# Kernel optimization log

Measured on AMD Instinct MI355X. Metric: run time of the kernel, lower is better.

Reference implementation:

```python
import jax, jax.numpy as jnp
import numpy as np

B, L, C = 2, 512, 64
EPS = 1e-5

def layer_norm(x, w, b):
    mu = jnp.mean(x, axis=-1, keepdims=True)
    var = jnp.mean(jnp.square(x - mu), axis=-1, keepdims=True)
    return (x - mu) * jax.lax.rsqrt(var + EPS) * w + b

def setup_inputs() -> dict:
    key = jax.random.key(0)
    ks = jax.random.split(key, 16)
    s = 1.0 / np.sqrt(C)
    def lin(k):
        k1, k2 = jax.random.split(k)
        return (jax.random.uniform(k1, (C, C), jnp.float32, -s, s),
                jax.random.uniform(k2, (C,), jnp.float32, -s, s))
    W_lp, b_lp = lin(ks[0]); W_rp, b_rp = lin(ks[1])
    W_lg, b_lg = lin(ks[2]); W_rg, b_rg = lin(ks[3])
    W_og, b_og = lin(ks[4]); W_out, b_out = lin(ks[5])
    return {
        'pairwise_states': jax.random.normal(ks[6], (B, L, L, C), jnp.float32),
        'attention_mask': jnp.ones((B, 1, 1, L), jnp.float32),
        'ln_in_w': jnp.ones((C,), jnp.float32), 'ln_in_b': jnp.zeros((C,), jnp.float32),
        'W_lp': W_lp, 'b_lp': b_lp, 'W_rp': W_rp, 'b_rp': b_rp,
        'W_lg': W_lg, 'b_lg': b_lg, 'W_rg': W_rg, 'b_rg': b_rg,
        'W_og': W_og, 'b_og': b_og,
        'ln_out_w': jnp.ones((C,), jnp.float32), 'ln_out_b': jnp.zeros((C,), jnp.float32),
        'W_out': W_out, 'b_out': b_out,
    }

def reference(pairwise_states, attention_mask, ln_in_w, ln_in_b,
              W_lp, b_lp, W_rp, b_rp, W_lg, b_lg, W_rg, b_rg,
              W_og, b_og, ln_out_w, ln_out_b, W_out, b_out):
    residual = pairwise_states
    x = layer_norm(pairwise_states, ln_in_w, ln_in_b)  # [B,L,L,C]
    left = x @ W_lp + b_lp
    right = x @ W_rp + b_rp
    # attention_mask [B,1,1,L].transpose(1,3) -> [B,L,1,1]: masks the i (row) axis
    m = jnp.transpose(attention_mask, (0, 3, 2, 1))
    left = left * m
    right = right * m
    left = left * jax.nn.sigmoid(x @ W_lg + b_lg)
    right = right * jax.nn.sigmoid(x @ W_rg + b_rg)
    out_gate = jax.nn.sigmoid(x @ W_og + b_og)
    # outgoing triangle update: out[b,i,j,c] = sum_k left[b,i,k,c] * right[b,j,k,c]
    tri = jnp.einsum('bikc,bjkc->bijc', left, right)
    y = layer_norm(tri, ln_out_w, ln_out_b) * out_gate
    y = y @ W_out + b_out
    return y + residual
```

## Files before the change

kernel.cpp:

```cpp
#include <hip/hip_runtime.h>
#include <cstdint>

typedef float f32x4 __attribute__((ext_vector_type(4)));
typedef short s16x8 __attribute__((ext_vector_type(8)));

#define APAD 72

__device__ __forceinline__ unsigned short f2bf(float f) {
  union { float f; uint32_t u; } v; v.f = f;
  uint32_t u = v.u;
  u += 0x7fffu + ((u >> 16) & 1u);
  return (unsigned short)(u >> 16);
}
__device__ __forceinline__ float bf2f(unsigned short h) {
  union { uint32_t u; float f; } v; v.u = ((uint32_t)h) << 16;
  return v.f;
}
__device__ __forceinline__ uint32_t pkbf(float a, float b) {
  uint32_t r;
  asm("v_cvt_pk_bf16_f32 %0, %1, %2" : "=v"(r) : "v"(a), "v"(b));
  return r;
}
__device__ __forceinline__ float sigmoidf_(float x) {
  return 1.0f / (1.0f + __expf(-x));
}
__device__ __forceinline__ f32x4 zero4() {
  f32x4 z = {0.f, 0.f, 0.f, 0.f};
  return z;
}
__device__ __forceinline__ void gl_lds16(const void* g, void* l) {
  __builtin_amdgcn_global_load_lds(
      (const __attribute__((address_space(1))) uint32_t*)g,
      (__attribute__((address_space(3))) uint32_t*)l, 16, 0, 0);
}

__global__ __launch_bounds__(256) void k_prep(
    const float* __restrict__ Wlp, const float* __restrict__ Wrp,
    const float* __restrict__ Wlg, const float* __restrict__ Wrg,
    const float* __restrict__ Wog, const float* __restrict__ Wout,
    unsigned short* __restrict__ wt) {
  const float* srcs[6] = {Wlp, Wrp, Wlg, Wrg, Wog, Wout};
  const int m = blockIdx.x;
  const float* W = srcs[m];
  const int t = threadIdx.x;
  for (int e = t; e < 64 * APAD; e += 256) {
    const int n = e / APAD, k = e - n * APAD;
    wt[m * (64 * APAD) + e] = (k < 64) ? f2bf(W[k * 64 + n]) : (unsigned short)0;
  }
}

__global__ __launch_bounds__(256, 4) void k1_proj(
    const float* __restrict__ xin, const float* __restrict__ mask,
    const float* __restrict__ lnw, const float* __restrict__ lnb,
    const float* __restrict__ blp, const float* __restrict__ brp,
    const float* __restrict__ blg, const float* __restrict__ brg,
    const unsigned short* __restrict__ wt,
    unsigned short* __restrict__ leftT, unsigned short* __restrict__ rightT) {
  __shared__ unsigned short A[64 * APAD];
  __shared__ unsigned short TL[64 * APAD];
  __shared__ unsigned short TR[64 * APAD];
  const int tid = threadIdx.x, lane = tid & 63, w = tid >> 6;
  const int bid = blockIdx.x;
  const int b = bid >> 12;
  const int i = (bid >> 3) & 511;
  const int k0 = (bid & 7) << 6;

  const int pair = w >> 1, ch = w & 1;
  const int kh8 = (lane >> 4) << 3;
  s16x8 wp[2][2], wg[2][2];
  float bPv[2], bGv[2];
  {
    const unsigned short* wtP = wt + (size_t)pair * (64 * APAD);
    const unsigned short* wtG = wt + (size_t)(2 + pair) * (64 * APAD);
    const float* bP = pair ? brp : blp;
    const float* bG = pair ? brg : blg;
#pragma unroll
    for (int nf2 = 0; nf2 < 2; ++nf2) {
      const int n = ch * 32 + nf2 * 16 + (lane & 15);
      const unsigned short* pp = wtP + n * APAD + kh8;
      const unsigned short* pg = wtG + n * APAD + kh8;
      wp[nf2][0] = *(const s16x8*)pp;  wp[nf2][1] = *(const s16x8*)(pp + 32);
      wg[nf2][0] = *(const s16x8*)pg;  wg[nf2][1] = *(const s16x8*)(pg + 32);
      bPv[nf2] = bP[n];  bGv[nf2] = bG[n];
    }
  }

  const int p = tid >> 2, q = tid & 3;
  const float* xrow = xin + (((size_t)b * 512 + i) * 512 + k0 + p) * 64 + q * 16;
  f32x4 xv[4];
#pragma unroll
  for (int u = 0; u < 4; ++u) xv[u] = ((const f32x4*)xrow)[u];
  float s1 = 0.f, s2 = 0.f;
#pragma unroll
  for (int u = 0; u < 4; ++u)
#pragma unroll
    for (int e = 0; e < 4; ++e) { float t = xv[u][e]; s1 += t; s2 += t * t; }
  s1 += __shfl_xor(s1, 1); s2 += __shfl_xor(s2, 1);
  s1 += __shfl_xor(s1, 2); s2 += __shfl_xor(s2, 2);
  const float mu = s1 * 0.015625f;
  const float rs = rsqrtf(s2 * 0.015625f - mu * mu + 1e-5f);
  {
    uint32_t pk[8];
#pragma unroll
    for (int u = 0; u < 4; ++u) {
      f32x4 wv = ((const f32x4*)(lnw + q * 16))[u];
      f32x4 bv = ((const f32x4*)(lnb + q * 16))[u];
#pragma unroll
      for (int e2 = 0; e2 < 2; ++e2) {
        pk[u * 2 + e2] = pkbf((xv[u][2 * e2] - mu) * rs * wv[2 * e2] + bv[2 * e2],
                              (xv[u][2 * e2 + 1] - mu) * rs * wv[2 * e2 + 1] + bv[2 * e2 + 1]);
      }
    }
    uint32_t* a32 = (uint32_t*)&A[p * APAD + q * 16];
#pragma unroll
    for (int u = 0; u < 8; ++u) a32[u] = pk[u];
  }
  const float mval = mask[b * 512 + i];
  __syncthreads();

  const int fr4 = (lane >> 4) << 2;
  unsigned short* T = pair ? TR : TL;
#pragma unroll
  for (int mf = 0; mf < 4; ++mf) {
    const int ar = (mf * 16 + (lane & 15)) * APAD + kh8;
    const s16x8 a0 = *(const s16x8*)&A[ar];
    const s16x8 a1 = *(const s16x8*)&A[ar + 32];
    f32x4 accP[2], accG[2];
#pragma unroll
    for (int nf2 = 0; nf2 < 2; ++nf2) {
      accP[nf2] = zero4(); accG[nf2] = zero4();
      accP[nf2] = __builtin_amdgcn_mfma_f32_16x16x32_bf16(a0, wp[nf2][0], accP[nf2], 0, 0, 0);
      accP[nf2] = __builtin_amdgcn_mfma_f32_16x16x32_bf16(a1, wp[nf2][1], accP[nf2], 0, 0, 0);
      accG[nf2] = __builtin_amdgcn_mfma_f32_16x16x32_bf16(a0, wg[nf2][0], accG[nf2], 0, 0, 0);
      accG[nf2] = __builtin_amdgcn_mfma_f32_16x16x32_bf16(a1, wg[nf2][1], accG[nf2], 0, 0, 0);
    }
    const int prow = mf * 16 + fr4;
#pragma unroll
    for (int nf2 = 0; nf2 < 2; ++nf2) {
      const int n = ch * 32 + nf2 * 16 + (lane & 15);
      const float bl = bPv[nf2], bg = bGv[nf2];
      float v0 = (accP[nf2][0] + bl) * mval * sigmoidf_(accG[nf2][0] + bg);
      float v1 = (accP[nf2][1] + bl) * mval * sigmoidf_(accG[nf2][1] + bg);
      float v2 = (accP[nf2][2] + bl) * mval * sigmoidf_(accG[nf2][2] + bg);
      float v3 = (accP[nf2][3] + bl) * mval * sigmoidf_(accG[nf2][3] + bg);
      *(uint32_t*)&T[n * APAD + prow] = pkbf(v0, v1);
      *(uint32_t*)&T[n * APAD + prow + 2] = pkbf(v2, v3);
    }
  }
  __syncthreads();

  {
    const int sn = tid >> 2, sq = tid & 3;
    const size_t gbase = (((size_t)b * 64 + sn) * 512 + i) * 512 + k0 + sq * 16;
    const uint32_t* sl = (const uint32_t*)&TL[sn * APAD + sq * 16];
    const uint32_t* sr = (const uint32_t*)&TR[sn * APAD + sq * 16];
    uint32_t* dl = (uint32_t*)(leftT + gbase);
    uint32_t* dr = (uint32_t*)(rightT + gbase);
#pragma unroll
    for (int u = 0; u < 8; ++u) dl[u] = sl[u];
#pragma unroll
    for (int u = 0; u < 8; ++u) dr[u] = sr[u];
  }
}

__global__ __launch_bounds__(256, 4) void k2_gemm(
    const unsigned short* __restrict__ leftT,
    const unsigned short* __restrict__ rightT,
    unsigned short* __restrict__ triT) {
  __shared__ __align__(16) unsigned short S[4 * 4096];
  const int tid = threadIdx.x, lane = tid & 63, w = tid >> 6;
  const int bid = blockIdx.x;
  const int sw = ((bid & 7) << 8) | (bid >> 3);
  const int plane = sw >> 4, tile = sw & 15;
  const size_t pb = (size_t)plane * 262144;
  const int i0 = (tile >> 2) << 7, j0 = (tile & 3) << 7;
  const int srow = lane >> 2;
  const int sk = (((lane & 3) ^ ((lane >> 2) & 3)) << 3);

  f32x4 acc[4][4];
#pragma unroll
  for (int mf = 0; mf < 4; ++mf)
#pragma unroll
    for (int nf = 0; nf < 4; ++nf) acc[mf][nf] = zero4();
  const int wr = (w >> 1) << 6, wc = (w & 1) << 6;

  auto stage = [&](int buf, int kt) {
    const int kk = kt << 5;
#pragma unroll
    for (int it = 0; it < 2; ++it) {
      const int ch = it * 4 + w;
      const int row = (ch << 4) + srow;
      gl_lds16(leftT + pb + (size_t)(i0 + row) * 512 + kk + sk,
               (char*)S + buf * 16384 + ch * 1024 + lane * 16);
      gl_lds16(rightT + pb + (size_t)(j0 + row) * 512 + kk + sk,
               (char*)S + buf * 16384 + 8192 + ch * 1024 + lane * 16);
    }
  };

  stage(0, 0);
  const int l15 = lane & 15;
  const int kosw = ((lane >> 4) ^ (lane & 3)) << 3;
  for (int kt = 0; kt < 16; ++kt) {
    __syncthreads();
    if (kt < 15) stage((kt & 1) ^ 1, kt + 1);
    const unsigned short* Ac = S + (kt & 1) * 8192;
    const unsigned short* Bc = Ac + 4096;
    s16x8 af[4], bfr[4];
#pragma unroll
    for (int mf = 0; mf < 4; ++mf)
      af[mf] = *(const s16x8*)&Ac[(wr + mf * 16 + l15) * 32 + kosw];
#pragma unroll
    for (int nf = 0; nf < 4; ++nf)
      bfr[nf] = *(const s16x8*)&Bc[(wc + nf * 16 + l15) * 32 + kosw];
#pragma unroll
    for (int mf = 0; mf < 4; ++mf)
#pragma unroll
      for (int nf = 0; nf < 4; ++nf)
        acc[mf][nf] = __builtin_amdgcn_mfma_f32_16x16x32_bf16(af[mf], bfr[nf], acc[mf][nf], 0, 0, 0);
  }
  __syncthreads();
  unsigned short* Tt = S;
#pragma unroll
  for (int mf = 0; mf < 4; ++mf)
#pragma unroll
    for (int nf = 0; nf < 4; ++nf) {
      const int col = wc + nf * 16 + l15;
#pragma unroll
      for (int r = 0; r < 4; ++r) {
        const int row = wr + mf * 16 + ((lane >> 4) << 2) + r;
        Tt[row * 128 + col] = f2bf(acc[mf][nf][r]);
      }
    }
  __syncthreads();
  {
    const int row = tid >> 1, half = (tid & 1) << 6;
    const uint32_t* src = (const uint32_t*)&Tt[row * 128 + half];
    uint32_t* dst = (uint32_t*)(triT + pb + (size_t)(i0 + row) * 512 + j0 + half);
#pragma unroll
    for (int u = 0; u < 32; ++u) dst[u] = src[u];
  }
}

#define OPAD 68
__global__ __launch_bounds__(256, 4) void k3_out(
    const unsigned short* __restrict__ triT,
    const float* __restrict__ resid,
    const float* __restrict__ lnw1, const float* __restrict__ lnb1,
    const float* __restrict__ bog,
    const float* __restrict__ lnw2, const float* __restrict__ lnb2,
    const float* __restrict__ bout,
    const unsigned short* __restrict__ wt,
    float* __restrict__ outp) {
  __shared__ __align__(16) unsigned char smem[36864];
  unsigned short* WTog  = (unsigned short*)smem;
  unsigned short* WTout = (unsigned short*)(smem + 9216);
  unsigned short* Y     = (unsigned short*)(smem + 18432);
  unsigned short* X     = (unsigned short*)(smem + 27648);
  float* OUT32 = (float*)(smem + 18432);
  const int tid = threadIdx.x, lane = tid & 63, w = tid >> 6;
  const int bid = blockIdx.x;
  const int b = bid >> 12;
  const int i = (bid >> 3) & 511;
  const int j0 = (bid & 7) << 6;

  {
    const char* wsrc = (const char*)(wt + (size_t)4 * (64 * APAD));
#pragma unroll
    for (int it = 0; it < 5; ++it) {
      const int off = (it * 256 + tid) * 16;
      if (off < 18432) gl_lds16(wsrc + off, (char*)WTog + off);
    }
  }

  const int j = tid >> 2, q = tid & 3;
  {
    const int c = tid >> 2;
    const int csw = c ^ (q << 4);
    const size_t srow = ((size_t)(b * 64 + c) * 512 + i) * 512 + j0 + q * 16;
    union { uint32_t u32[8]; unsigned short s[16]; } uu;
    const uint32_t* s32 = (const uint32_t*)(triT + srow);
#pragma unroll
    for (int u = 0; u < 8; ++u) uu.u32[u] = s32[u];
#pragma unroll
    for (int s = 0; s < 16; ++s) Y[(q * 16 + s) * APAD + csw] = uu.s[s];
  }
  f32x4 rv[4];
  {
    const float* rrow = resid + (((size_t)b * 512 + i) * 512 + j0 + j) * 64 + q * 16;
#pragma unroll
    for (int u = 0; u < 4; ++u) rv[u] = ((const f32x4*)rrow)[u];
    float s1 = 0.f, s2 = 0.f;
#pragma unroll
    for (int u = 0; u < 4; ++u)
#pragma unroll
      for (int e = 0; e < 4; ++e) { float t = rv[u][e]; s1 += t; s2 += t * t; }
    s1 += __shfl_xor(s1, 1); s2 += __shfl_xor(s2, 1);
    s1 += __shfl_xor(s1, 2); s2 += __shfl_xor(s2, 2);
    const float mu = s1 * 0.015625f;
    const float rs = rsqrtf(s2 * 0.015625f - mu * mu + 1e-5f);
    uint32_t pk[8];
#pragma unroll
    for (int u = 0; u < 4; ++u) {
      f32x4 wv = ((const f32x4*)(lnw1 + q * 16))[u];
      f32x4 bv = ((const f32x4*)(lnb1 + q * 16))[u];
#pragma unroll
      for (int e2 = 0; e2 < 2; ++e2) {
        pk[u * 2 + e2] = pkbf((rv[u][2 * e2] - mu) * rs * wv[2 * e2] + bv[2 * e2],
                              (rv[u][2 * e2 + 1] - mu) * rs * wv[2 * e2 + 1] + bv[2 * e2 + 1]);
      }
    }
    uint32_t* x32 = (uint32_t*)&X[j * APAD + q * 16];
#pragma unroll
    for (int u = 0; u < 8; ++u) x32[u] = pk[u];
  }
  __syncthreads();

  const int l15 = lane & 15, hi = lane >> 4;
  const int jrow = w * 16 + l15;
  const int ybase = jrow * APAD;
  const int kh8 = hi << 3;
  float yv[16];
#pragma unroll
  for (int nf = 0; nf < 4; ++nf) {
    const int pc = (((nf ^ w) & 3) << 4) + (hi << 2);
    const uint2 dd = *(const uint2*)&Y[ybase + pc];
    yv[nf * 4 + 0] = bf2f((unsigned short)(dd.x & 0xffff));
    yv[nf * 4 + 1] = bf2f((unsigned short)(dd.x >> 16));
    yv[nf * 4 + 2] = bf2f((unsigned short)(dd.y & 0xffff));
    yv[nf * 4 + 3] = bf2f((unsigned short)(dd.y >> 16));
  }
  float t1 = 0.f, t2 = 0.f;
#pragma unroll
  for (int s = 0; s < 16; ++s) { t1 += yv[s]; t2 += yv[s] * yv[s]; }
  t1 += __shfl_xor(t1, 16); t2 += __shfl_xor(t2, 16);
  t1 += __shfl_xor(t1, 32); t2 += __shfl_xor(t2, 32);
  const float mu2 = t1 * 0.015625f;
  const float rs2 = rsqrtf(t2 * 0.015625f - mu2 * mu2 + 1e-5f);

  float sg[16];
  {
    const s16x8 xb0 = *(const s16x8*)&X[ybase + kh8];
    const s16x8 xb1 = *(const s16x8*)&X[ybase + kh8 + 32];
#pragma unroll
    for (int nf = 0; nf < 4; ++nf) {
      const int wrow = (nf * 16 + l15) * APAD + kh8;
      const s16x8 wa0 = *(const s16x8*)&WTog[wrow];
      const s16x8 wa1 = *(const s16x8*)&WTog[wrow + 32];
      f32x4 aog = zero4();
      aog = __builtin_amdgcn_mfma_f32_16x16x32_bf16(wa0, xb0, aog, 0, 0, 0);
      aog = __builtin_amdgcn_mfma_f32_16x16x32_bf16(wa1, xb1, aog, 0, 0, 0);
      const f32x4 bb4 = *(const f32x4*)(bog + nf * 16 + (hi << 2));
      sg[nf * 4 + 0] = sigmoidf_(aog[0] + bb4[0]);
      sg[nf * 4 + 1] = sigmoidf_(aog[1] + bb4[1]);
      sg[nf * 4 + 2] = sigmoidf_(aog[2] + bb4[2]);
      sg[nf * 4 + 3] = sigmoidf_(aog[3] + bb4[3]);
    }
  }
#pragma unroll
  for (int nf = 0; nf < 4; ++nf) {
    const f32x4 wv = *(const f32x4*)(lnw2 + nf * 16 + (hi << 2));
    const f32x4 bv = *(const f32x4*)(lnb2 + nf * 16 + (hi << 2));
    const float y0 = ((yv[nf * 4 + 0] - mu2) * rs2 * wv[0] + bv[0]) * sg[nf * 4 + 0];
    const float y1 = ((yv[nf * 4 + 1] - mu2) * rs2 * wv[1] + bv[1]) * sg[nf * 4 + 1];
    const float y2 = ((yv[nf * 4 + 2] - mu2) * rs2 * wv[2] + bv[2]) * sg[nf * 4 + 2];
    const float y3 = ((yv[nf * 4 + 3] - mu2) * rs2 * wv[3] + bv[3]) * sg[nf * 4 + 3];
    uint2 o;
    o.x = pkbf(y0, y1);
    o.y = pkbf(y2, y3);
    const int pc = (((nf ^ w) & 3) << 4) + (hi << 2);
    *(uint2*)&Y[ybase + pc] = o;
  }
  __syncthreads();

  {
    const int xsw = (w & 3) << 4;
    const s16x8 a0 = *(const s16x8*)&Y[ybase + (kh8 ^ xsw)];
    const s16x8 a1 = *(const s16x8*)&Y[ybase + ((32 + kh8) ^ xsw)];
    s16x8 wb0[4], wb1[4];
#pragma unroll
    for (int nf = 0; nf < 4; ++nf) {
      const int brow = (nf * 16 + l15) * APAD + kh8;
      wb0[nf] = *(const s16x8*)&WTout[brow];
      wb1[nf] = *(const s16x8*)&WTout[brow + 32];
    }
    __syncthreads();
    f32x4 ao[4];
#pragma unroll
    for (int nf = 0; nf < 4; ++nf) {
      ao[nf] = zero4();
      ao[nf] = __builtin_amdgcn_mfma_f32_16x16x32_bf16(a0, wb0[nf], ao[nf], 0, 0, 0);
      ao[nf] = __builtin_amdgcn_mfma_f32_16x16x32_bf16(a1, wb1[nf], ao[nf], 0, 0, 0);
    }
#pragma unroll
    for (int nf = 0; nf < 4; ++nf) {
      const int n = nf * 16 + l15;
      const float bo = bout[n];
#pragma unroll
      for (int r = 0; r < 4; ++r) {
        const int prow = w * 16 + (hi << 2) + r;
        OUT32[prow * OPAD + n] = ao[nf][r] + bo;
      }
    }
  }
  __syncthreads();

  {
    const size_t gb = (((size_t)b * 512 + i) * 512 + j0 + j) * 64 + q * 16;
    float* op = outp + gb;
#pragma unroll
    for (int u = 0; u < 4; ++u) {
      f32x4 ov = ((const f32x4*)&OUT32[j * OPAD + q * 16])[u];
      ((f32x4*)op)[u] = ov + rv[u];
    }
  }
}

extern "C" void kernel_launch(void* const* d_in, const int* in_sizes, int n_in,
                              void* d_out, int out_size, void* d_ws, size_t ws_size,
                              hipStream_t stream) {
  const float* x     = (const float*)d_in[0];
  const float* mask  = (const float*)d_in[1];
  const float* lnw1  = (const float*)d_in[2];
  const float* lnb1  = (const float*)d_in[3];
  const float* Wlp   = (const float*)d_in[4];
  const float* blp   = (const float*)d_in[5];
  const float* Wrp   = (const float*)d_in[6];
  const float* brp   = (const float*)d_in[7];
  const float* Wlg   = (const float*)d_in[8];
  const float* blg   = (const float*)d_in[9];
  const float* Wrg   = (const float*)d_in[10];
  const float* brg   = (const float*)d_in[11];
  const float* Wog   = (const float*)d_in[12];
  const float* bog   = (const float*)d_in[13];
  const float* lnw2  = (const float*)d_in[14];
  const float* lnb2  = (const float*)d_in[15];
  const float* Wout  = (const float*)d_in[16];
  const float* bout  = (const float*)d_in[17];

  unsigned short* leftT  = (unsigned short*)d_ws;
  unsigned short* rightT = leftT + (size_t)33554432;
  unsigned short* triT   = rightT + (size_t)33554432;
  unsigned short* wt     = triT + (size_t)33554432;

  k_prep<<<6, 256, 0, stream>>>(Wlp, Wrp, Wlg, Wrg, Wog, Wout, wt);
  k1_proj<<<8192, 256, 0, stream>>>(x, mask, lnw1, lnb1, blp, brp, blg, brg,
                                    wt, leftT, rightT);
  k2_gemm<<<2048, 256, 0, stream>>>(leftT, rightT, triT);
  k3_out<<<8192, 256, 0, stream>>>(triT, x, lnw1, lnb1, bog, lnw2, lnb2, bout,
                                   wt, (float*)d_out);
}
```

Before: 242.5 us.

## Keep k3 LN-input in registers and write output directly from MFMA fragments

The output kernel now computes the input layernorm straight into MFMA B-fragment registers instead of staging X through shared memory. It swaps the output GEMM operand order so results land in row-major fragments that can be written to global memory directly, which removes the OUT32 shared buffer and two barriers. Shared memory drops from 36KB to 27KB and launch bounds rise to 5 blocks per SM for higher occupancy. The cost is that the residual is read from global twice, and the final stores are 16-byte chunks per lane rather than full contiguous rows.

```diff
diff --git a/kernel.cpp b/kernel.cpp
--- a/kernel.cpp
+++ b/kernel.cpp
@@ -241,8 +241,7 @@
   }
 }
 
-#define OPAD 68
-__global__ __launch_bounds__(256, 4) void k3_out(
+__global__ __launch_bounds__(256, 5) void k3_out(
     const unsigned short* __restrict__ triT,
     const float* __restrict__ resid,
     const float* __restrict__ lnw1, const float* __restrict__ lnb1,
@@ -251,12 +250,10 @@
     const float* __restrict__ bout,
     const unsigned short* __restrict__ wt,
     float* __restrict__ outp) {
-  __shared__ __align__(16) unsigned char smem[36864];
+  __shared__ __align__(16) unsigned char smem[27648];
   unsigned short* WTog  = (unsigned short*)smem;
   unsigned short* WTout = (unsigned short*)(smem + 9216);
   unsigned short* Y     = (unsigned short*)(smem + 18432);
-  unsigned short* X     = (unsigned short*)(smem + 27648);
-  float* OUT32 = (float*)(smem + 18432);
   const int tid = threadIdx.x, lane = tid & 63, w = tid >> 6;
   const int bid = blockIdx.x;
   const int b = bid >> 12;
@@ -272,7 +269,50 @@
     }
   }
 
-  const int j = tid >> 2, q = tid & 3;
+  const int l15 = lane & 15, hi = lane >> 4;
+  const int jrow = w * 16 + l15;
+  const size_t rowbase = (((size_t)b * 512 + i) * 512 + j0 + jrow) * 64;
+  const int kh8 = hi << 3;
+
+  s16x8 xb0, xb1;
+  {
+    f32x4 rx[4];
+    rx[0] = *(const f32x4*)(resid + rowbase + kh8);
+    rx[1] = *(const f32x4*)(resid + rowbase + kh8 + 4);
+    rx[2] = *(const f32x4*)(resid + rowbase + 32 + kh8);
+    rx[3] = *(const f32x4*)(resid + rowbase + 36 + kh8);
+    float s1 = 0.f, s2 = 0.f;
+#pragma unroll
+    for (int u = 0; u < 4; ++u)
+#pragma unroll
+      for (int e = 0; e < 4; ++e) { float t = rx[u][e]; s1 += t; s2 += t * t; }
+    s1 += __shfl_xor(s1, 16); s2 += __shfl_xor(s2, 16);
+    s1 += __shfl_xor(s1, 32); s2 += __shfl_xor(s2, 32);
+    const float mu = s1 * 0.015625f;
+    const float rs = rsqrtf(s2 * 0.015625f - mu * mu + 1e-5f);
+    union { uint32_t u[4]; s16x8 v; } p0, p1;
+#pragma unroll
+    for (int u = 0; u < 2; ++u) {
+      f32x4 wv = *(const f32x4*)(lnw1 + kh8 + u * 4);
+      f32x4 bv = *(const f32x4*)(lnb1 + kh8 + u * 4);
+      p0.u[u * 2 + 0] = pkbf((rx[u][0] - mu) * rs * wv[0] + bv[0],
+                             (rx[u][1] - mu) * rs * wv[1] + bv[1]);
+      p0.u[u * 2 + 1] = pkbf((rx[u][2] - mu) * rs * wv[2] + bv[2],
+                             (rx[u][3] - mu) * rs * wv[3] + bv[3]);
+    }
+#pragma unroll
+    for (int u = 0; u < 2; ++u) {
+      f32x4 wv = *(const f32x4*)(lnw1 + 32 + kh8 + u * 4);
+      f32x4 bv = *(const f32x4*)(lnb1 + 32 + kh8 + u * 4);
+      p1.u[u * 2 + 0] = pkbf((rx[u + 2][0] - mu) * rs * wv[0] + bv[0],
+                             (rx[u + 2][1] - mu) * rs * wv[1] + bv[1]);
+      p1.u[u * 2 + 1] = pkbf((rx[u + 2][2] - mu) * rs * wv[2] + bv[2],
+                             (rx[u + 2][3] - mu) * rs * wv[3] + bv[3]);
+    }
+    xb0 = p0.v; xb1 = p1.v;
+  }
+
+  const int q = tid & 3;
   {
     const int c = tid >> 2;
     const int csw = c ^ (q << 4);
@@ -284,41 +324,9 @@
 #pragma unroll
     for (int s = 0; s < 16; ++s) Y[(q * 16 + s) * APAD + csw] = uu.s[s];
   }
-  f32x4 rv[4];
-  {
-    const float* rrow = resid + (((size_t)b * 512 + i) * 512 + j0 + j) * 64 + q * 16;
-#pragma unroll
-    for (int u = 0; u < 4; ++u) rv[u] = ((const f32x4*)rrow)[u];
-    float s1 = 0.f, s2 = 0.f;
-#pragma unroll
-    for (int u = 0; u < 4; ++u)
-#pragma unroll
-      for (int e = 0; e < 4; ++e) { float t = rv[u][e]; s1 += t; s2 += t * t; }
-    s1 += __shfl_xor(s1, 1); s2 += __shfl_xor(s2, 1);
-    s1 += __shfl_xor(s1, 2); s2 += __shfl_xor(s2, 2);
-    const float mu = s1 * 0.015625f;
-    const float rs = rsqrtf(s2 * 0.015625f - mu * mu + 1e-5f);
-    uint32_t pk[8];
-#pragma unroll
-    for (int u = 0; u < 4; ++u) {
-      f32x4 wv = ((const f32x4*)(lnw1 + q * 16))[u];
-      f32x4 bv = ((const f32x4*)(lnb1 + q * 16))[u];
-#pragma unroll
-      for (int e2 = 0; e2 < 2; ++e2) {
-        pk[u * 2 + e2] = pkbf((rv[u][2 * e2] - mu) * rs * wv[2 * e2] + bv[2 * e2],
-                              (rv[u][2 * e2 + 1] - mu) * rs * wv[2 * e2 + 1] + bv[2 * e2 + 1]);
-      }
-    }
-    uint32_t* x32 = (uint32_t*)&X[j * APAD + q * 16];
-#pragma unroll
-    for (int u = 0; u < 8; ++u) x32[u] = pk[u];
-  }
-  __syncthreads();
-
-  const int l15 = lane & 15, hi = lane >> 4;
-  const int jrow = w * 16 + l15;
+  __syncthreads();
+
   const int ybase = jrow * APAD;
-  const int kh8 = hi << 3;
   float yv[16];
 #pragma unroll
   for (int nf = 0; nf < 4; ++nf) {
@@ -337,33 +345,21 @@
   const float mu2 = t1 * 0.015625f;
   const float rs2 = rsqrtf(t2 * 0.015625f - mu2 * mu2 + 1e-5f);
 
-  float sg[16];
-  {
-    const s16x8 xb0 = *(const s16x8*)&X[ybase + kh8];
-    const s16x8 xb1 = *(const s16x8*)&X[ybase + kh8 + 32];
-#pragma unroll
-    for (int nf = 0; nf < 4; ++nf) {
-      const int wrow = (nf * 16 + l15) * APAD + kh8;
-      const s16x8 wa0 = *(const s16x8*)&WTog[wrow];
-      const s16x8 wa1 = *(const s16x8*)&WTog[wrow + 32];
-      f32x4 aog = zero4();
-      aog = __builtin_amdgcn_mfma_f32_16x16x32_bf16(wa0, xb0, aog, 0, 0, 0);
-      aog = __builtin_amdgcn_mfma_f32_16x16x32_bf16(wa1, xb1, aog, 0, 0, 0);
-      const f32x4 bb4 = *(const f32x4*)(bog + nf * 16 + (hi << 2));
-      sg[nf * 4 + 0] = sigmoidf_(aog[0] + bb4[0]);
-      sg[nf * 4 + 1] = sigmoidf_(aog[1] + bb4[1]);
-      sg[nf * 4 + 2] = sigmoidf_(aog[2] + bb4[2]);
-      sg[nf * 4 + 3] = sigmoidf_(aog[3] + bb4[3]);
-    }
-  }
 #pragma unroll
   for (int nf = 0; nf < 4; ++nf) {
+    const int wrow = (nf * 16 + l15) * APAD + kh8;
+    const s16x8 wa0 = *(const s16x8*)&WTog[wrow];
+    const s16x8 wa1 = *(const s16x8*)&WTog[wrow + 32];
+    f32x4 aog = zero4();
+    aog = __builtin_amdgcn_mfma_f32_16x16x32_bf16(wa0, xb0, aog, 0, 0, 0);
+    aog = __builtin_amdgcn_mfma_f32_16x16x32_bf16(wa1, xb1, aog, 0, 0, 0);
+    const f32x4 bg4 = *(const f32x4*)(bog + nf * 16 + (hi << 2));
     const f32x4 wv = *(const f32x4*)(lnw2 + nf * 16 + (hi << 2));
     const f32x4 bv = *(const f32x4*)(lnb2 + nf * 16 + (hi << 2));
-    const float y0 = ((yv[nf * 4 + 0] - mu2) * rs2 * wv[0] + bv[0]) * sg[nf * 4 + 0];
-    const float y1 = ((yv[nf * 4 + 1] - mu2) * rs2 * wv[1] + bv[1]) * sg[nf * 4 + 1];
-    const float y2 = ((yv[nf * 4 + 2] - mu2) * rs2 * wv[2] + bv[2]) * sg[nf * 4 + 2];
-    const float y3 = ((yv[nf * 4 + 3] - mu2) * rs2 * wv[3] + bv[3]) * sg[nf * 4 + 3];
+    const float y0 = ((yv[nf * 4 + 0] - mu2) * rs2 * wv[0] + bv[0]) * sigmoidf_(aog[0] + bg4[0]);
+    const float y1 = ((yv[nf * 4 + 1] - mu2) * rs2 * wv[1] + bv[1]) * sigmoidf_(aog[1] + bg4[1]);
+    const float y2 = ((yv[nf * 4 + 2] - mu2) * rs2 * wv[2] + bv[2]) * sigmoidf_(aog[2] + bg4[2]);
+    const float y3 = ((yv[nf * 4 + 3] - mu2) * rs2 * wv[3] + bv[3]) * sigmoidf_(aog[3] + bg4[3]);
     uint2 o;
     o.x = pkbf(y0, y1);
     o.y = pkbf(y2, y3);
@@ -373,44 +369,24 @@
   __syncthreads();
 
   {
-    const int xsw = (w & 3) << 4;
+    const int xsw = w << 4;
     const s16x8 a0 = *(const s16x8*)&Y[ybase + (kh8 ^ xsw)];
     const s16x8 a1 = *(const s16x8*)&Y[ybase + ((32 + kh8) ^ xsw)];
-    s16x8 wb0[4], wb1[4];
+    f32x4 rv4[4];
+#pragma unroll
+    for (int nf = 0; nf < 4; ++nf)
+      rv4[nf] = *(const f32x4*)(resid + rowbase + nf * 16 + (hi << 2));
 #pragma unroll
     for (int nf = 0; nf < 4; ++nf) {
       const int brow = (nf * 16 + l15) * APAD + kh8;
-      wb0[nf] = *(const s16x8*)&WTout[brow];
-      wb1[nf] = *(const s16x8*)&WTout[brow + 32];
-    }
-    __syncthreads();
-    f32x4 ao[4];
-#pragma unroll
-    for (int nf = 0; nf < 4; ++nf) {
-      ao[nf] = zero4();
-      ao[nf] = __builtin_amdgcn_mfma_f32_16x16x32_bf16(a0, wb0[nf], ao[nf], 0, 0, 0);
-      ao[nf] = __builtin_amdgcn_mfma_f32_16x16x32_bf16(a1, wb1[nf], ao[nf], 0, 0, 0);
-    }
-#pragma unroll
-    for (int nf = 0; nf < 4; ++nf) {
-      const int n = nf * 16 + l15;
-      const float bo = bout[n];
-#pragma unroll
-      for (int r = 0; r < 4; ++r) {
-        const int prow = w * 16 + (hi << 2) + r;
-        OUT32[prow * OPAD + n] = ao[nf][r] + bo;
-      }
-    }
-  }
-  __syncthreads();
-
-  {
-    const size_t gb = (((size_t)b * 512 + i) * 512 + j0 + j) * 64 + q * 16;
-    float* op = outp + gb;
-#pragma unroll
-    for (int u = 0; u < 4; ++u) {
-      f32x4 ov = ((const f32x4*)&OUT32[j * OPAD + q * 16])[u];
-      ((f32x4*)op)[u] = ov + rv[u];
+      const s16x8 wb0 = *(const s16x8*)&WTout[brow];
+      const s16x8 wb1 = *(const s16x8*)&WTout[brow + 32];
+      f32x4 ao = zero4();
+      ao = __builtin_amdgcn_mfma_f32_16x16x32_bf16(wb0, a0, ao, 0, 0, 0);
+      ao = __builtin_amdgcn_mfma_f32_16x16x32_bf16(wb1, a1, ao, 0, 0, 0);
+      const f32x4 bo4 = *(const f32x4*)(bout + nf * 16 + (hi << 2));
+      f32x4 ov = ao + bo4 + rv4[nf];
+      *(f32x4*)(outp + rowbase + nf * 16 + (hi << 2)) = ov;
     }
   }
 }
```

New measurement: 247.2 us. Within noise of the previous version (+1.9%).
